# Optimization experiments

Hardware: AMD Instinct MI355X
Metric: run time of the kernel (lower is better)

The kernel has to match this reference:

```python
import jax, jax.numpy as jnp
import numpy as np

V_THRESH = 0.3

@jax.custom_vjp
def spike(x):
    return (x > 0).astype(x.dtype)

def _spike_fwd(x):
    return spike(x), x

def _spike_bwd(x, g):
    # rectangular straight-through surrogate gradient (pass grad where |x| < 0.5)
    return (g * (jnp.abs(x) < 0.5).astype(g.dtype),)

spike.defvjp(_spike_fwd, _spike_bwd)


def setup_inputs() -> dict:
    key = jax.random.key(0)
    B, T, H = 128, 2048, 128
    k1, = jax.random.split(key, 1)
    x_seq = jax.random.normal(k1, (B, T, H), dtype=jnp.float32)
    v0 = jnp.zeros((B, H), dtype=jnp.float32)
    z0 = jnp.zeros((B, H), dtype=jnp.float32)
    decay_raw = jnp.zeros((H,), dtype=jnp.float32)  # nn.initializers.constant(0.0)
    return {"x_seq": x_seq, "v0": v0, "z0": z0, "decay_raw": decay_raw}


def reference(x_seq, v0, z0, decay_raw):
    # LIF recurrence: v_t = v_{t-1} * decay * (1 - z_{t-1}) + x_t ; z_t = spike(v_t - v_thresh)
    decay = jax.nn.sigmoid(decay_raw)  # (H,)

    def step(carry, x_t):
        v, z = carry
        v = v * decay * (1.0 - z) + x_t
        z_out = spike(v - V_THRESH)
        return (v, z_out), z_out

    x_tb = jnp.swapaxes(x_seq, 0, 1)  # [T, B, H] for lax.scan over time
    (_, _), spk_tb = jax.lax.scan(step, (v0, z0), x_tb)
    return jnp.swapaxes(spk_tb, 0, 1)  # [B, T, H]
```

## Files before the change

kernel.cpp:

```cpp
#include <hip/hip_runtime.h>
#include <math.h>


constexpr int Bdim = 128;
constexpr int Tdim = 2048;
constexpr int Hdim = 128;
constexpr int HW   = 64;
constexpr int U    = 128;
constexpr int NBUF = 4;
constexpr int NTILE = Tdim / U;
constexpr float VTH = 0.3f;

typedef const __attribute__((address_space(1))) void* gptr_t;
typedef __attribute__((address_space(3))) void* lptr_t;

#define BAR()     asm volatile("s_barrier" ::: "memory")
#define WAITV16() asm volatile("s_waitcnt vmcnt(16)" ::: "memory")
#define WAITV0()  asm volatile("s_waitcnt vmcnt(0)" ::: "memory")
#define WAITL0()  asm volatile("s_waitcnt lgkmcnt(0)" ::: "memory")

__global__ __launch_bounds__(256) void lif_kernel(
    const float* __restrict__ x,
    const float* __restrict__ v0,
    const float* __restrict__ z0,
    const float* __restrict__ decay_raw,
    float* __restrict__ out)
{
    __shared__ float lds[NBUF][U][HW];

    const int tid  = threadIdx.x;
    const int wave = tid >> 6;
    const int lane = tid & 63;
    const int blk  = blockIdx.x;
    const int b    = blk >> 1;
    const int h0   = (blk & 1) * HW;

    const float* xbase = x   + (size_t)b * Tdim * Hdim + h0;
    float*       obase = out + (size_t)b * Tdim * Hdim + h0;

    const int sub = (lane >> 4) * Hdim + (lane & 15) * 4;

    auto fill = [&](int tile, int buf) {
        const float* g = xbase + (size_t)tile * U * Hdim + sub;
        #pragma unroll
        for (int q = 0; q < 16; ++q) {
            const int jj = (wave - 1) * 16 + q;
            __builtin_amdgcn_global_load_lds(
                (gptr_t)(const void*)(g + (size_t)(4 * jj) * Hdim),
                (lptr_t)(void*)&lds[buf][4 * jj][0],
                16, 0, 0);
        }
    };

    auto flush = [&](int tile, int buf) {
        #pragma unroll
        for (int s = 0; s < 32; ++s) {
            const int row = 4 * s + (lane >> 4);
            const int col = (lane & 15) * 4;
            const float4 vv = *(const float4*)&lds[buf][row][col];
            *(float4*)(obase + (size_t)(tile * U + row) * Hdim + col) = vv;
        }
    };

    float decay = 0.f, v = 0.f, z = 0.f;
    if (wave == 0) {
        decay = 1.0f / (1.0f + expf(-decay_raw[h0 + lane]));
        v = v0[b * Hdim + h0 + lane];
        z = z0[b * Hdim + h0 + lane];
    } else if (wave <= 2) {
        fill(0, 0);
        fill(1, 1);
        WAITV16();
    }
    BAR();

    for (int k = 0; k < NTILE; ++k) {
        if (wave == 0) {
            const int cb = k & 3;
            float xa[16], xb[16];
            #pragma unroll
            for (int j = 0; j < 16; ++j) xa[j] = lds[cb][j][lane];
            #pragma unroll
            for (int g = 0; g < 8; ++g) {
                if (g < 7) {
                    #pragma unroll
                    for (int j = 0; j < 16; ++j) {
                        const float t = lds[cb][(g + 1) * 16 + j][lane];
                        if (g & 1) xa[j] = t; else xb[j] = t;
                    }
                }
                #pragma unroll
                for (int j = 0; j < 16; ++j) {
                    const float xv = (g & 1) ? xb[j] : xa[j];
                    const float vd = v * decay;
                    v = ((z > 0.5f) ? 0.0f : vd) + xv;
                    z = (v > VTH) ? 1.0f : 0.0f;
                    lds[cb][g * 16 + j][lane] = z;
                }
            }
            WAITL0();
        } else if (wave <= 2) {
            if (k + 2 < NTILE) {
                fill(k + 2, (k + 2) & 3);
                WAITV16();
            } else {
                WAITV0();
            }
        } else {
            if (k >= 1) flush(k - 1, (k - 1) & 3);
        }
        BAR();
    }
    if (wave == 3) flush(NTILE - 1, (NTILE - 1) & 3);
}

extern "C" void kernel_launch(void* const* d_in, const int* in_sizes, int n_in,
                              void* d_out, int out_size, void* d_ws, size_t ws_size,
                              hipStream_t stream) {
    const float* x         = (const float*)d_in[0];
    const float* v0        = (const float*)d_in[1];
    const float* z0        = (const float*)d_in[2];
    const float* decay_raw = (const float*)d_in[3];
    float* out = (float*)d_out;

    lif_kernel<<<Bdim * Hdim / HW, 256, 0, stream>>>(x, v0, z0, decay_raw, out);
}
```

Baseline: 247.0 us.

## Load inputs straight to registers in compute wave, use helper wave for L2 prefetch

The compute wave now reads x directly from global memory into a 4-slot register ring, three groups of 16 timesteps ahead, instead of through LDS buffers filled by async global-to-LDS loads. The second wave reads tiles two ahead and sums them into a dummy accumulator purely to warm the cache, then writes the spike tiles out of a double-buffered LDS area. The block shrinks from four waves to two and LDS use is halved. The trade-off is that x is read twice, and the serial recurrence now waits on global or L2 latency instead of LDS reads.

New measurement: 244.9 us. No clear change (-0.9%).

```diff
diff --git a/kernel.cpp b/kernel.cpp
--- a/kernel.cpp
+++ b/kernel.cpp
@@ -7,26 +7,20 @@
 constexpr int Hdim = 128;
 constexpr int HW   = 64;
 constexpr int U    = 128;
-constexpr int NBUF = 4;
 constexpr int NTILE = Tdim / U;
 constexpr float VTH = 0.3f;
 
-typedef const __attribute__((address_space(1))) void* gptr_t;
-typedef __attribute__((address_space(3))) void* lptr_t;
+#define BAR()    asm volatile("s_barrier" ::: "memory")
+#define WAITL0() asm volatile("s_waitcnt lgkmcnt(0)" ::: "memory")
 
-#define BAR()     asm volatile("s_barrier" ::: "memory")
-#define WAITV16() asm volatile("s_waitcnt vmcnt(16)" ::: "memory")
-#define WAITV0()  asm volatile("s_waitcnt vmcnt(0)" ::: "memory")
-#define WAITL0()  asm volatile("s_waitcnt lgkmcnt(0)" ::: "memory")
-
-__global__ __launch_bounds__(256) void lif_kernel(
+__global__ __launch_bounds__(128) void lif_kernel(
     const float* __restrict__ x,
     const float* __restrict__ v0,
     const float* __restrict__ z0,
     const float* __restrict__ decay_raw,
     float* __restrict__ out)
 {
-    __shared__ float lds[NBUF][U][HW];
+    __shared__ float zs[2][U][HW];
 
     const int tid  = threadIdx.x;
     const int wave = tid >> 6;
@@ -38,80 +32,78 @@
     const float* xbase = x   + (size_t)b * Tdim * Hdim + h0;
     float*       obase = out + (size_t)b * Tdim * Hdim + h0;
 
-    const int sub = (lane >> 4) * Hdim + (lane & 15) * 4;
+    if (wave == 0) {
+        const float* xl = xbase + lane;
+        const float decay = 1.0f / (1.0f + expf(-decay_raw[h0 + lane]));
+        float v = v0[b * Hdim + h0 + lane];
+        float z = z0[b * Hdim + h0 + lane];
 
-    auto fill = [&](int tile, int buf) {
-        const float* g = xbase + (size_t)tile * U * Hdim + sub;
+        float xq[4][16];
         #pragma unroll
-        for (int q = 0; q < 16; ++q) {
-            const int jj = (wave - 1) * 16 + q;
-            __builtin_amdgcn_global_load_lds(
-                (gptr_t)(const void*)(g + (size_t)(4 * jj) * Hdim),
-                (lptr_t)(void*)&lds[buf][4 * jj][0],
-                16, 0, 0);
-        }
-    };
+        for (int q = 0; q < 3; ++q)
+            #pragma unroll
+            for (int j = 0; j < 16; ++j)
+                xq[q][j] = xl[(size_t)(q * 16 + j) * Hdim];
 
-    auto flush = [&](int tile, int buf) {
-        #pragma unroll
-        for (int s = 0; s < 32; ++s) {
-            const int row = 4 * s + (lane >> 4);
-            const int col = (lane & 15) * 4;
-            const float4 vv = *(const float4*)&lds[buf][row][col];
-            *(float4*)(obase + (size_t)(tile * U + row) * Hdim + col) = vv;
-        }
-    };
-
-    float decay = 0.f, v = 0.f, z = 0.f;
-    if (wave == 0) {
-        decay = 1.0f / (1.0f + expf(-decay_raw[h0 + lane]));
-        v = v0[b * Hdim + h0 + lane];
-        z = z0[b * Hdim + h0 + lane];
-    } else if (wave <= 2) {
-        fill(0, 0);
-        fill(1, 1);
-        WAITV16();
-    }
-    BAR();
-
-    for (int k = 0; k < NTILE; ++k) {
-        if (wave == 0) {
-            const int cb = k & 3;
-            float xa[16], xb[16];
-            #pragma unroll
-            for (int j = 0; j < 16; ++j) xa[j] = lds[cb][j][lane];
+        for (int k = 0; k < NTILE; ++k) {
+            float* zcol = &zs[k & 1][0][lane];
             #pragma unroll
             for (int g = 0; g < 8; ++g) {
-                if (g < 7) {
+                if (k * 8 + g + 3 < 8 * NTILE) {
+                    const size_t t3 = (size_t)(k * 8 + g + 3) * 16;
                     #pragma unroll
-                    for (int j = 0; j < 16; ++j) {
-                        const float t = lds[cb][(g + 1) * 16 + j][lane];
-                        if (g & 1) xa[j] = t; else xb[j] = t;
-                    }
+                    for (int j = 0; j < 16; ++j)
+                        xq[(g + 3) & 3][j] = xl[(t3 + j) * Hdim];
                 }
                 #pragma unroll
                 for (int j = 0; j < 16; ++j) {
-                    const float xv = (g & 1) ? xb[j] : xa[j];
+                    const float xv = xq[g & 3][j];
                     const float vd = v * decay;
                     v = ((z > 0.5f) ? 0.0f : vd) + xv;
                     z = (v > VTH) ? 1.0f : 0.0f;
-                    lds[cb][g * 16 + j][lane] = z;
+                    zcol[(g * 16 + j) * HW] = z;
                 }
             }
             WAITL0();
-        } else if (wave <= 2) {
+            BAR();
+        }
+    } else {
+        const int col = (lane & 15) * 4;
+        const int rb  = lane >> 4;
+        const int sub = rb * Hdim + col;
+        float4 acc = make_float4(0.f, 0.f, 0.f, 0.f);
+
+        for (int k = 0; k < NTILE; ++k) {
             if (k + 2 < NTILE) {
-                fill(k + 2, (k + 2) & 3);
-                WAITV16();
-            } else {
-                WAITV0();
+                const float* p = xbase + (size_t)(k + 2) * U * Hdim + sub;
+                #pragma unroll
+                for (int s = 0; s < 32; ++s) {
+                    const float4 t = *(const float4*)(p + (size_t)(4 * s) * Hdim);
+                    acc.x += t.x; acc.y += t.y; acc.z += t.z; acc.w += t.w;
+                }
             }
-        } else {
-            if (k >= 1) flush(k - 1, (k - 1) & 3);
+            if (k >= 1) {
+                const int tt = k - 1;
+                #pragma unroll
+                for (int s = 0; s < 32; ++s) {
+                    const int row = 4 * s + rb;
+                    const float4 vv = *(const float4*)&zs[tt & 1][row][col];
+                    *(float4*)(obase + (size_t)(tt * U + row) * Hdim + col) = vv;
+                }
+            }
+            BAR();
         }
-        BAR();
+        {
+            const int tt = NTILE - 1;
+            #pragma unroll
+            for (int s = 0; s < 32; ++s) {
+                const int row = 4 * s + rb;
+                const float4 vv = *(const float4*)&zs[tt & 1][row][col];
+                *(float4*)(obase + (size_t)(tt * U + row) * Hdim + col) = vv;
+            }
+        }
+        asm volatile("" :: "v"(acc.x), "v"(acc.y), "v"(acc.z), "v"(acc.w));
     }
-    if (wave == 3) flush(NTILE - 1, (NTILE - 1) & 3);
 }
 
 extern "C" void kernel_launch(void* const* d_in, const int* in_sizes, int n_in,
@@ -123,5 +115,5 @@
     const float* decay_raw = (const float*)d_in[3];
     float* out = (float*)d_out;
 
-    lif_kernel<<<Bdim * Hdim / HW, 256, 0, stream>>>(x, v0, z0, decay_raw, out);
+    lif_kernel<<<Bdim * Hdim / HW, 128, 0, stream>>>(x, v0, z0, decay_raw, out);
 }
```
